# Kernel optimization log

Hardware: AMD Instinct MI355X
Metric: run time of the kernel (lower is better)

## Reference

```python
import jax, jax.numpy as jnp
import numpy as np

B, L, D_MODEL, H = 2, 2048, 2048, 16
HD = D_MODEL // H  # 128 head dim
EPS = 1e-6


def rms_norm(x, scale):
    # float32 RMSNorm over last dim, per Flux QKNorm
    x32 = x.astype(jnp.float32)
    rrms = jax.lax.rsqrt(jnp.mean(x32 * x32, axis=-1, keepdims=True) + EPS)
    return (x32 * rrms) * scale


def apply_rope(xq, xk, freqs_cis):
    # xq, xk: [B, L, H, D]; freqs_cis: [1, L, 1, D/2, 2, 2]
    shp = xq.shape
    xq_ = xq.astype(jnp.float32).reshape(*shp[:-1], -1, 1, 2)
    xk_ = xk.astype(jnp.float32).reshape(*shp[:-1], -1, 1, 2)
    xq_out = freqs_cis[..., 0] * xq_[..., 0] + freqs_cis[..., 1] * xq_[..., 1]
    xk_out = freqs_cis[..., 0] * xk_[..., 0] + freqs_cis[..., 1] * xk_[..., 1]
    return xq_out.reshape(shp).astype(xq.dtype), xk_out.reshape(shp).astype(xk.dtype)


def setup_inputs() -> dict:
    key = jax.random.key(0)
    k1, k2, k3, k4 = jax.random.split(key, 4)
    x = jax.random.normal(k1, (B, L, D_MODEL), dtype=jnp.float32)
    pe = jax.random.normal(k2, (1, L, 1, HD // 2, 2, 2), dtype=jnp.float32)
    w_qkv = jax.random.normal(k3, (D_MODEL, 3 * D_MODEL), dtype=jnp.float32) * (D_MODEL ** -0.5)
    w_proj = jax.random.normal(k4, (D_MODEL, D_MODEL), dtype=jnp.float32) * (D_MODEL ** -0.5)
    q_scale = jnp.ones((HD,), dtype=jnp.float32)
    k_scale = jnp.ones((HD,), dtype=jnp.float32)
    return {"x": x, "pe": pe, "w_qkv": w_qkv, "w_proj": w_proj,
            "q_scale": q_scale, "k_scale": k_scale}


def reference(x, pe, w_qkv, w_proj, q_scale, k_scale):
    qkv = x @ w_qkv                                  # [B, L, 3*H*D]
    qkv = qkv.reshape(B, L, 3, H, HD)
    q, k, v = qkv[:, :, 0], qkv[:, :, 1], qkv[:, :, 2]  # [B, L, H, D]
    # QK RMSNorm (cast back to v's dtype, per QKNorm.forward)
    q = rms_norm(q, q_scale).astype(v.dtype)
    k = rms_norm(k, k_scale).astype(v.dtype)
    # RoPE
    q, k = apply_rope(q, k, pe)
    # non-causal SDPA
    scale = HD ** -0.5
    scores = jnp.einsum('blhd,bmhd->bhlm', q, k) * scale
    attn = jax.nn.softmax(scores, axis=-1)
    out = jnp.einsum('bhlm,bmhd->blhd', attn, v)     # [B, L, H, D]
    out = out.reshape(B, L, H * HD)
    return out @ w_proj
```

## Files before the change

kernel.cpp:

```cpp
#include <hip/hip_runtime.h>

typedef unsigned short u16;
typedef __bf16 bf16x8 __attribute__((ext_vector_type(8)));
typedef float f32x4 __attribute__((ext_vector_type(4)));

#define DEV static __device__ __forceinline__

constexpr int Bc  = 2;
constexpr int Lc  = 2048;
constexpr int Dc  = 2048;
constexpr int Hc  = 16;
constexpr int HDc = 128;
constexpr int Mc  = Bc * Lc;
constexpr int N3c = 3 * Dc;

DEV u16 f2bf(float f) {
  unsigned u = __builtin_bit_cast(unsigned, f);
  u += 0x7fffu + ((u >> 16) & 1u);
  return (u16)(u >> 16);
}
DEV float bf2f(u16 h) { return __builtin_bit_cast(float, ((unsigned)h) << 16); }

DEV void load16(const void* g, void* l) {
  __builtin_amdgcn_global_load_lds(
      (__attribute__((address_space(1))) void*)(g),
      (__attribute__((address_space(3))) void*)(l), 16, 0, 0);
}

__global__ __launch_bounds__(256) void k_prep(const float* __restrict__ x,
                                              const float* __restrict__ w_qkv,
                                              const float* __restrict__ w_proj,
                                              u16* __restrict__ xb,
                                              u16* __restrict__ wqkvT,
                                              u16* __restrict__ wpT) {
  __shared__ u16 t[128 * 136];
  int bid = blockIdx.x;
  int tid = threadIdx.x;
  if (bid < 4096) {
    int i = bid * 256 + tid;
    const float4* s = (const float4*)x;
    float4 a = s[2 * i], b = s[2 * i + 1];
    uint4 o;
    o.x = f2bf(a.x) | ((unsigned)f2bf(a.y) << 16);
    o.y = f2bf(a.z) | ((unsigned)f2bf(a.w) << 16);
    o.z = f2bf(b.x) | ((unsigned)f2bf(b.y) << 16);
    o.w = f2bf(b.z) | ((unsigned)f2bf(b.w) << 16);
    ((uint4*)xb)[i] = o;
    return;
  }
  const float* src;
  u16* dst;
  int tiles_c;
  long ss;
  if (bid < 4096 + 768) {
    int bx = bid - 4096;
    src = w_qkv; dst = wqkvT; tiles_c = 48; ss = N3c;
    int tr = bx / tiles_c, tc = bx % tiles_c;
    src += (long)tr * 128 * ss + tc * 128;
    dst += (long)(tc * 128) * Dc + tr * 128;
  } else {
    int bx = bid - 4864;
    src = w_proj; dst = wpT; tiles_c = 16; ss = Dc;
    int tr = bx / tiles_c, tc = bx % tiles_c;
    src += (long)tr * 128 * ss + tc * 128;
    dst += (long)(tc * 128) * Dc + tr * 128;
  }
#pragma unroll
  for (int p = 0; p < 16; p++) {
    int r = p * 8 + (tid >> 5);
    int c4 = (tid & 31) * 4;
    float4 v = *(const float4*)(src + (long)r * ss + c4);
    t[(c4 + 0) * 136 + r] = f2bf(v.x);
    t[(c4 + 1) * 136 + r] = f2bf(v.y);
    t[(c4 + 2) * 136 + r] = f2bf(v.z);
    t[(c4 + 3) * 136 + r] = f2bf(v.w);
  }
  __syncthreads();
#pragma unroll
  for (int p = 0; p < 8; p++) {
    int c = p * 16 + (tid >> 4);
    int r8 = (tid & 15) * 8;
    uint4 v = *(const uint4*)&t[c * 136 + r8];
    *(uint4*)(dst + (long)c * Dc + r8) = v;
  }
}

__global__ __launch_bounds__(256) void k_vtrans(const u16* __restrict__ qkvb,
                                                u16* __restrict__ Vt) {
  int lt = blockIdx.x;
  int bh = blockIdx.y;
  int b = bh >> 4, h = bh & 15;
  const u16* s = qkvb + (long)(b * Lc + lt * 128) * N3c + 2 * Dc + h * HDc;
  u16* d = Vt + (long)bh * HDc * Lc + lt * 128;
  __shared__ u16 t[128 * 136];
  int tid = threadIdx.x;
#pragma unroll
  for (int p = 0; p < 8; p++) {
    int r = p * 16 + (tid >> 4);
    int c = (tid & 15) * 8;
    uint4 v = *(const uint4*)(s + (long)r * N3c + c);
    const u16* pv = (const u16*)&v;
#pragma unroll
    for (int j = 0; j < 8; j++) t[(c + j) * 136 + r] = pv[j];
  }
  __syncthreads();
#pragma unroll
  for (int p = 0; p < 8; p++) {
    int c = p * 16 + (tid >> 4);
    int r8 = (tid & 15) * 8;
    *(uint4*)(d + (long)c * Lc + r8) = *(const uint4*)&t[c * 136 + r8];
  }
}

DEV void cstore(float* p, float v) { *p = v; }
DEV void cstore(u16* p, float v) { *p = f2bf(v); }

template <typename OT>
__global__ __launch_bounds__(512, 2) void k_gemm2p(const u16* __restrict__ A,
                                                   const u16* __restrict__ Bt,
                                                   OT* __restrict__ C,
                                                   int M, int N, int K,
                                                   int RM, int RC) {
  __shared__ __align__(16) u16 sA[3][128 * 64];
  __shared__ __align__(16) u16 sB[3][256 * 64];

  int nb = N >> 8;
  int x = blockIdx.x & 7;
  int u = blockIdx.x >> 3;
  int rcr = nb / RC;
  int brow = (x / rcr) * RM + (u % RM);
  int bcol = (x % rcr) * RC + (u / RM);

  int tid = threadIdx.x, w = tid >> 6, lane = tid & 63;
  int wm = w >> 2, wn = w & 3;
  int quad = lane >> 4, l15 = lane & 15;
  int lr = lane >> 3, lc = lane & 7;
  int NT = K >> 6;

  const u16* Ag = A + (long)(brow * 128 + w * 8 + lr) * K + (lc ^ lr) * 8;
  const u16* Bg = Bt + (long)(bcol * 256 + w * 8 + lr) * K + (lc ^ lr) * 8;

  f32x4 acc[4][4] = {};
  bf16x8 a[4][2];
  bf16x8 b[4][2];

#define STAGE_A(c, t)                                                          \
  if ((t) < NT) {                                                              \
    _Pragma("unroll") for (int j = 0; j < 2; j++)                              \
        load16(Ag + (long)(j * 64) * K + (long)(t) * 64,                       \
               &sA[c][(j * 64 + w * 8) * 64]);                                 \
  }
#define STAGE_B(c, t)                                                          \
  if ((t) < NT) {                                                              \
    _Pragma("unroll") for (int j = 0; j < 4; j++)                              \
        load16(Bg + (long)(j * 64) * K + (long)(t) * 64,                       \
               &sB[c][(j * 64 + w * 8) * 64]);                                 \
  }
#define LDAB(c)                                                                \
  _Pragma("unroll") for (int mi = 0; mi < 4; mi++) {                           \
    int r = wm * 64 + mi * 16 + l15;                                           \
    _Pragma("unroll") for (int kk = 0; kk < 2; kk++)                           \
        a[mi][kk] =                                                            \
        *(const bf16x8*)&sA[c][r * 64 + (((kk * 4 + quad) ^ (r & 7)) << 3)];   \
  }                                                                            \
  _Pragma("unroll") for (int fi = 0; fi < 4; fi++) {                           \
    int rn = wn * 64 + fi * 16 + l15;                                          \
    _Pragma("unroll") for (int kk = 0; kk < 2; kk++)                           \
        b[fi][kk] =                                                            \
        *(const bf16x8*)&sB[c][rn * 64 + (((kk * 4 + quad) ^ (rn & 7)) << 3)]; \
  }
#define MFMAH(qm)                                                              \
  _Pragma("unroll") for (int mi = 0; mi < 2; mi++)                             \
  _Pragma("unroll") for (int fi = 0; fi < 4; fi++)                             \
  _Pragma("unroll") for (int kk = 0; kk < 2; kk++)                             \
      acc[(qm)*2 + mi][fi] = __builtin_amdgcn_mfma_f32_16x16x32_bf16(          \
          a[(qm)*2 + mi][kk], b[fi][kk], acc[(qm)*2 + mi][fi], 0, 0, 0);
#define BAR() __builtin_amdgcn_s_barrier()
#define LGKM0()                                      \
  asm volatile("s_waitcnt lgkmcnt(0)" ::: "memory"); \
  __builtin_amdgcn_sched_barrier(0)

#define TILE(c, t)                                                             \
  {                                                                            \
    LDAB(c);                                                                   \
    LGKM0();                                                                   \
    __builtin_amdgcn_s_setprio(1);                                             \
    MFMAH(0);                                                                  \
    __builtin_amdgcn_s_setprio(0);                                             \
    BAR();                        \
    STAGE_A(c, (t) + 3);                                                       \
    STAGE_B(c, (t) + 3);                                                       \
    __builtin_amdgcn_s_setprio(1);                                             \
    MFMAH(1);                                                                  \
    __builtin_amdgcn_s_setprio(0);                                             \
    if ((t) < NT - 3) {                                                        \
      asm volatile("s_waitcnt vmcnt(12)" ::: "memory");                        \
    } else if ((t) == NT - 3) {                                                \
      asm volatile("s_waitcnt vmcnt(6)" ::: "memory");                         \
    } else {                                                                   \
      asm volatile("s_waitcnt vmcnt(0)" ::: "memory");                         \
    }                                                                          \
    __builtin_amdgcn_sched_barrier(0);                                         \
    BAR();                          \
  }

  STAGE_A(0, 0);
  STAGE_B(0, 0);
  STAGE_A(1, 1);
  STAGE_B(1, 1);
  STAGE_A(2, 2);
  STAGE_B(2, 2);
  asm volatile("s_waitcnt vmcnt(12)" ::: "memory");
  __builtin_amdgcn_sched_barrier(0);
  BAR();

  int kt = 0;
  for (; kt + 2 < NT; kt += 3) {
    TILE(0, kt);
    TILE(1, kt + 1);
    TILE(2, kt + 2);
  }
  if (kt < NT) { TILE(0, kt); }
  if (kt + 1 < NT) { TILE(1, kt + 1); }

  long orow = (long)brow * 128 + wm * 64;
  int ocol = bcol * 256 + wn * 64;
#pragma unroll
  for (int mi = 0; mi < 4; mi++)
#pragma unroll
    for (int fi = 0; fi < 4; fi++)
#pragma unroll
      for (int r = 0; r < 4; r++)
        cstore(&C[(orow + mi * 16 + quad * 4 + r) * (long)N + ocol + fi * 16 + l15],
               acc[mi][fi][r]);
#undef STAGE_A
#undef STAGE_B
#undef LDAB
#undef MFMAH
#undef BAR
#undef LGKM0
#undef TILE
}

__global__ __launch_bounds__(256) void k_rmsrope(const u16* __restrict__ qkvb,
                                                 const float* __restrict__ pe,
                                                 const float* __restrict__ qsc,
                                                 const float* __restrict__ ksc,
                                                 u16* __restrict__ Qr,
                                                 u16* __restrict__ Kr) {
  int row = blockIdx.x;
  int l = row & (Lc - 1);
  int b = row >> 11;
  int tid = threadIdx.x;
  int h = tid >> 4, s16 = tid & 15;
  int d0 = s16 * 8;
  const u16* qp = qkvb + (long)row * N3c + h * HDc + d0;
  uint4 qv = *(const uint4*)qp;
  uint4 kv = *(const uint4*)(qp + Dc);
  const u16* qu = (const u16*)&qv;
  const u16* ku = (const u16*)&kv;
  float q[8], k[8];
#pragma unroll
  for (int j = 0; j < 8; j++) {
    q[j] = bf2f(qu[j]);
    k[j] = bf2f(ku[j]);
  }
  float sq = 0.f, sk = 0.f;
#pragma unroll
  for (int j = 0; j < 8; j++) {
    sq += q[j] * q[j];
    sk += k[j] * k[j];
  }
#pragma unroll
  for (int m = 1; m < 16; m <<= 1) {
    sq += __shfl_xor(sq, m);
    sk += __shfl_xor(sk, m);
  }
  float rq = rsqrtf(sq * (1.f / HDc) + 1e-6f);
  float rk = rsqrtf(sk * (1.f / HDc) + 1e-6f);
  float qs8[8], ks8[8];
  *(float4*)&qs8[0] = *(const float4*)(qsc + d0);
  *(float4*)&qs8[4] = *(const float4*)(qsc + d0 + 4);
  *(float4*)&ks8[0] = *(const float4*)(ksc + d0);
  *(float4*)&ks8[4] = *(const float4*)(ksc + d0 + 4);
#pragma unroll
  for (int j = 0; j < 8; j++) {
    q[j] *= rq * qs8[j];
    k[j] *= rk * ks8[j];
  }
  float e[16];
  const float* pep = pe + (long)l * 256 + s16 * 16;
#pragma unroll
  for (int j = 0; j < 4; j++) *(float4*)&e[j * 4] = *(const float4*)(pep + j * 4);
  float qo[8], ko[8];
#pragma unroll
  for (int p = 0; p < 4; p++) {
    float e00 = e[p * 4 + 0], e01 = e[p * 4 + 1];
    float e10 = e[p * 4 + 2], e11 = e[p * 4 + 3];
    qo[2 * p]     = e00 * q[2 * p] + e01 * q[2 * p + 1];
    qo[2 * p + 1] = e10 * q[2 * p] + e11 * q[2 * p + 1];
    ko[2 * p]     = e00 * k[2 * p] + e01 * k[2 * p + 1];
    ko[2 * p + 1] = e10 * k[2 * p] + e11 * k[2 * p + 1];
  }
  constexpr float RS = 0.08838834764831845f;
  uint4 oq, ok;
  oq.x = f2bf(qo[0] * RS) | ((unsigned)f2bf(qo[1] * RS) << 16);
  oq.y = f2bf(qo[2] * RS) | ((unsigned)f2bf(qo[3] * RS) << 16);
  oq.z = f2bf(qo[4] * RS) | ((unsigned)f2bf(qo[5] * RS) << 16);
  oq.w = f2bf(qo[6] * RS) | ((unsigned)f2bf(qo[7] * RS) << 16);
  ok.x = f2bf(ko[0]) | ((unsigned)f2bf(ko[1]) << 16);
  ok.y = f2bf(ko[2]) | ((unsigned)f2bf(ko[3]) << 16);
  ok.z = f2bf(ko[4]) | ((unsigned)f2bf(ko[5]) << 16);
  ok.w = f2bf(ko[6]) | ((unsigned)f2bf(ko[7]) << 16);
  long o = (((long)(b * Hc + h)) * Lc + l) * HDc + d0;
  *(uint4*)(Qr + o) = oq;
  *(uint4*)(Kr + o) = ok;
}

__global__ __launch_bounds__(256, 3) void k_attn(const u16* __restrict__ Qr,
                                                 const u16* __restrict__ Kr,
                                                 const u16* __restrict__ Vt,
                                                 u16* __restrict__ Ao) {
  __shared__ u16 smem[24576];
  u16* sQ = smem;
  u16* sK = smem + 8192;
  u16* sV = smem + 16384;
  u16* sP = sQ;
  int bx = blockIdx.x;
  int bh = (bx & 7) | ((bx >> 8) << 3);
  int lt = (bx >> 3) & 31;
  const u16* Qg = Qr + ((long)bh * Lc + lt * 64) * HDc;
  const u16* Kg = Kr + (long)bh * Lc * HDc;
  const u16* Vg = Vt + (long)bh * HDc * Lc;
  int tid = threadIdx.x, w = tid >> 6, lane = tid & 63;
  int quad = lane >> 4, l15 = lane & 15;
  int wsl = w >> 1, wsm = w & 1;
  int wd = w >> 1, wl2 = w & 1;

#pragma unroll
  for (int i = 0; i < 4; i++) {
    int r = i * 16 + w * 4 + quad;
    int gch = l15 ^ (r & 15);
    load16(Qg + (long)r * HDc + gch * 8, sQ + (i * 16 + w * 4) * 128);
  }
  __syncthreads();
  bf16x8 qf[2][4];
#pragma unroll
  for (int mi = 0; mi < 2; mi++) {
    int l = wsl * 32 + mi * 16 + l15;
#pragma unroll
    for (int kk = 0; kk < 4; kk++)
      qf[mi][kk] = *(const bf16x8*)&sQ[l * 128 + (((kk * 4 + quad) ^ l15) << 3)];
  }

  f32x4 o[4][2] = {};
  float rs[8] = {};
  for (int t = 0; t < 32; t++) {
    int m0 = t * 64;
    __syncthreads();
#pragma unroll
    for (int i = 0; i < 4; i++) {
      int r = i * 16 + w * 4 + quad;
      int gch = l15 ^ (r & 15);
      load16(Kg + ((long)(m0 + r)) * HDc + gch * 8, sK + (i * 16 + w * 4) * 128);
    }
#pragma unroll
    for (int i = 0; i < 4; i++) {
      int r = i * 32 + w * 8 + (lane >> 3);
      int gch = (lane & 7) ^ (r & 7);
      load16(Vg + (long)r * Lc + m0 + gch * 8, sV + (i * 32 + w * 8) * 64);
    }
    __syncthreads();
    f32x4 s[2][2] = {};
#pragma unroll
    for (int kk = 0; kk < 4; kk++) {
      bf16x8 bk[2];
#pragma unroll
      for (int ni = 0; ni < 2; ni++) {
        int m = wsm * 32 + ni * 16 + l15;
        bk[ni] = *(const bf16x8*)&sK[m * 128 + (((kk * 4 + quad) ^ l15) << 3)];
      }
#pragma unroll
      for (int mi = 0; mi < 2; mi++)
#pragma unroll
        for (int ni = 0; ni < 2; ni++)
          s[mi][ni] =
              __builtin_amdgcn_mfma_f32_16x16x32_bf16(qf[mi][kk], bk[ni], s[mi][ni], 0, 0, 0);
    }
#pragma unroll
    for (int mi = 0; mi < 2; mi++)
#pragma unroll
      for (int ni = 0; ni < 2; ni++) {
        int pc = wsm * 32 + ni * 16 + l15;
#pragma unroll
        for (int r = 0; r < 4; r++) {
          int pr = wsl * 32 + mi * 16 + quad * 4 + r;
          float p = __expf(s[mi][ni][r]);
          rs[mi * 4 + r] += p;
          unsigned u = __builtin_bit_cast(unsigned, p) + 0x8000u;
          sP[pr * 64 + ((((pc >> 3) ^ (pr & 7)) << 3) | (pc & 7))] = (u16)(u >> 16);
        }
      }
    __syncthreads();
#pragma unroll
    for (int kk = 0; kk < 2; kk++) {
      bf16x8 av[4], bp[2];
#pragma unroll
      for (int mi = 0; mi < 4; mi++) {
        int d = wd * 64 + mi * 16 + l15;
        av[mi] = *(const bf16x8*)&sV[d * 64 + (((kk * 4 + quad) ^ (d & 7)) << 3)];
      }
#pragma unroll
      for (int ni = 0; ni < 2; ni++) {
        int l = wl2 * 32 + ni * 16 + l15;
        bp[ni] = *(const bf16x8*)&sP[l * 64 + (((kk * 4 + quad) ^ (l & 7)) << 3)];
      }
#pragma unroll
      for (int mi = 0; mi < 4; mi++)
#pragma unroll
        for (int ni = 0; ni < 2; ni++)
          o[mi][ni] =
              __builtin_amdgcn_mfma_f32_16x16x32_bf16(av[mi], bp[ni], o[mi][ni], 0, 0, 0);
    }
  }
  __syncthreads();
  float* red  = (float*)sK;
  float* rsum = (float*)sV;
#pragma unroll
  for (int mi = 0; mi < 2; mi++)
#pragma unroll
    for (int r = 0; r < 4; r++) {
      int l = wsl * 32 + mi * 16 + quad * 4 + r;
      red[l * 33 + wsm * 16 + l15] = rs[mi * 4 + r];
    }
  __syncthreads();
  if (tid < 64) {
    float a = 0.f;
#pragma unroll
    for (int j = 0; j < 32; j++) a += red[tid * 33 + j];
    rsum[tid] = a;
  }
  __syncthreads();
  int b = bh >> 4, h = bh & 15;
#pragma unroll
  for (int ni = 0; ni < 2; ni++) {
    int l = wl2 * 32 + ni * 16 + l15;
    float inv = 1.f / rsum[l];
    long rowb = ((long)(b * Lc + lt * 64 + l)) * Dc + h * HDc;
#pragma unroll
    for (int mi = 0; mi < 4; mi++) {
      int d = wd * 64 + mi * 16 + quad * 4;
      ushort4 pk;
      pk.x = f2bf(o[mi][ni][0] * inv);
      pk.y = f2bf(o[mi][ni][1] * inv);
      pk.z = f2bf(o[mi][ni][2] * inv);
      pk.w = f2bf(o[mi][ni][3] * inv);
      *(ushort4*)(Ao + rowb + d) = pk;
    }
  }
}

extern "C" void kernel_launch(void* const* d_in, const int* in_sizes, int n_in,
                              void* d_out, int out_size, void* d_ws, size_t ws_size,
                              hipStream_t stream) {
  const float* x      = (const float*)d_in[0];
  const float* pe     = (const float*)d_in[1];
  const float* w_qkv  = (const float*)d_in[2];
  const float* w_proj = (const float*)d_in[3];
  const float* qs     = (const float*)d_in[4];
  const float* ks     = (const float*)d_in[5];
  float* out = (float*)d_out;
  char* ws = (char*)d_ws;

  u16* xb    = (u16*)(ws);
  u16* wqkvT = (u16*)(ws + 16777216);
  u16* wpT   = (u16*)(ws + 41943040);
  u16* qkvb  = (u16*)(ws + 50331648);
  u16* Qr    = (u16*)(ws + 100663296);
  u16* Kr    = (u16*)(ws + 117440512);
  u16* Vtw   = (u16*)(ws + 134217728);
  u16* Ao    = (u16*)(ws + 150994944);

  k_prep<<<5120, 256, 0, stream>>>(x, w_qkv, w_proj, xb, wqkvT, wpT);
  k_gemm2p<u16><<<32 * 24, 512, 0, stream>>>(xb, wqkvT, qkvb, Mc, N3c, Dc, 16, 6);
  k_rmsrope<<<Mc, 256, 0, stream>>>(qkvb, pe, qs, ks, Qr, Kr);
  k_vtrans<<<dim3(16, 32), 256, 0, stream>>>(qkvb, Vtw);
  k_attn<<<32 * 32, 256, 0, stream>>>(Qr, Kr, Vtw, Ao);
  k_gemm2p<float><<<32 * 8, 512, 0, stream>>>(Ao, wpT, out, Mc, Dc, Dc, 8, 4);
}
```

Baseline: 408.7 us.

## Double-buffer GEMM register fragments to overlap LDS reads with MFMA

Restructures the GEMM main loop so the LDS-to-register fragment loads for the next k-tile are issued while the MFMAs for the current tile run, using two register fragment sets. There is now one barrier per tile instead of two, and the global-to-LDS staging is issued right after that barrier. The goal is to hide LDS read latency and cut barrier stalls. The cost is roughly double the fragment register footprint, which may lower occupancy or cause spills. The tail handling also assumes the tile count parity fits the two-step loop.

```diff
diff --git a/kernel.cpp b/kernel.cpp
--- a/kernel.cpp
+++ b/kernel.cpp
@@ -141,87 +141,90 @@
   const u16* Bg = Bt + (long)(bcol * 256 + w * 8 + lr) * K + (lc ^ lr) * 8;
 
   f32x4 acc[4][4] = {};
-  bf16x8 a[4][2];
-  bf16x8 b[4][2];
-
-#define STAGE_A(c, t)                                                          \
+  bf16x8 a0[4][2], b0[4][2];
+  bf16x8 a1[4][2], b1[4][2];
+
+#define STAGE(c, t)                                                            \
   if ((t) < NT) {                                                              \
     _Pragma("unroll") for (int j = 0; j < 2; j++)                              \
         load16(Ag + (long)(j * 64) * K + (long)(t) * 64,                       \
                &sA[c][(j * 64 + w * 8) * 64]);                                 \
-  }
-#define STAGE_B(c, t)                                                          \
-  if ((t) < NT) {                                                              \
     _Pragma("unroll") for (int j = 0; j < 4; j++)                              \
         load16(Bg + (long)(j * 64) * K + (long)(t) * 64,                       \
                &sB[c][(j * 64 + w * 8) * 64]);                                 \
   }
-#define LDAB(c)                                                                \
+#define LDAB(c, ar, br)                                                        \
   _Pragma("unroll") for (int mi = 0; mi < 4; mi++) {                           \
     int r = wm * 64 + mi * 16 + l15;                                           \
     _Pragma("unroll") for (int kk = 0; kk < 2; kk++)                           \
-        a[mi][kk] =                                                            \
+        ar[mi][kk] =                                                           \
         *(const bf16x8*)&sA[c][r * 64 + (((kk * 4 + quad) ^ (r & 7)) << 3)];   \
   }                                                                            \
   _Pragma("unroll") for (int fi = 0; fi < 4; fi++) {                           \
     int rn = wn * 64 + fi * 16 + l15;                                          \
     _Pragma("unroll") for (int kk = 0; kk < 2; kk++)                           \
-        b[fi][kk] =                                                            \
+        br[fi][kk] =                                                           \
         *(const bf16x8*)&sB[c][rn * 64 + (((kk * 4 + quad) ^ (rn & 7)) << 3)]; \
   }
-#define MFMAH(qm)                                                              \
-  _Pragma("unroll") for (int mi = 0; mi < 2; mi++)                             \
+#define MFMAALL(ar, br)                                                        \
+  _Pragma("unroll") for (int mi = 0; mi < 4; mi++)                             \
   _Pragma("unroll") for (int fi = 0; fi < 4; fi++)                             \
   _Pragma("unroll") for (int kk = 0; kk < 2; kk++)                             \
-      acc[(qm)*2 + mi][fi] = __builtin_amdgcn_mfma_f32_16x16x32_bf16(          \
-          a[(qm)*2 + mi][kk], b[fi][kk], acc[(qm)*2 + mi][fi], 0, 0, 0);
+      acc[mi][fi] = __builtin_amdgcn_mfma_f32_16x16x32_bf16(                   \
+          ar[mi][kk], br[fi][kk], acc[mi][fi], 0, 0, 0);
+#define SB() __builtin_amdgcn_sched_barrier(0)
 #define BAR() __builtin_amdgcn_s_barrier()
-#define LGKM0()                                      \
-  asm volatile("s_waitcnt lgkmcnt(0)" ::: "memory"); \
-  __builtin_amdgcn_sched_barrier(0)
-
-#define TILE(c, t)                                                             \
+#define WAITV(n) asm volatile("s_waitcnt vmcnt(" #n ")" ::: "memory")
+#define WAITL0() asm volatile("s_waitcnt lgkmcnt(0)" ::: "memory")
+
+#define TILE_BODY(tt, sbuf, rbuf, arC, brC, arN, brN, vkeep)                   \
   {                                                                            \
-    LDAB(c);                                                                   \
-    LGKM0();                                                                   \
+    WAITV(vkeep);                                                              \
+    SB();                                                                      \
+    BAR();                                                                     \
+    SB();                                                                      \
+    STAGE(sbuf, (tt) + 3);                                                     \
+    LDAB(rbuf, arN, brN);                                                      \
     __builtin_amdgcn_s_setprio(1);                                             \
-    MFMAH(0);                                                                  \
+    MFMAALL(arC, brC);                                                         \
     __builtin_amdgcn_s_setprio(0);                                             \
-    BAR();                        \
-    STAGE_A(c, (t) + 3);                                                       \
-    STAGE_B(c, (t) + 3);                                                       \
-    __builtin_amdgcn_s_setprio(1);                                             \
-    MFMAH(1);                                                                  \
-    __builtin_amdgcn_s_setprio(0);                                             \
-    if ((t) < NT - 3) {                                                        \
-      asm volatile("s_waitcnt vmcnt(12)" ::: "memory");                        \
-    } else if ((t) == NT - 3) {                                                \
-      asm volatile("s_waitcnt vmcnt(6)" ::: "memory");                         \
-    } else {                                                                   \
-      asm volatile("s_waitcnt vmcnt(0)" ::: "memory");                         \
-    }                                                                          \
-    __builtin_amdgcn_sched_barrier(0);                                         \
-    BAR();                          \
-  }
-
-  STAGE_A(0, 0);
-  STAGE_B(0, 0);
-  STAGE_A(1, 1);
-  STAGE_B(1, 1);
-  STAGE_A(2, 2);
-  STAGE_B(2, 2);
-  asm volatile("s_waitcnt vmcnt(12)" ::: "memory");
-  __builtin_amdgcn_sched_barrier(0);
+    WAITL0();                                                                  \
+  }
+
+  STAGE(0, 0);
+  STAGE(1, 1);
+  STAGE(2, 2);
+  WAITV(12);
+  SB();
   BAR();
-
-  int kt = 0;
-  for (; kt + 2 < NT; kt += 3) {
-    TILE(0, kt);
-    TILE(1, kt + 1);
-    TILE(2, kt + 2);
-  }
-  if (kt < NT) { TILE(0, kt); }
-  if (kt + 1 < NT) { TILE(1, kt + 1); }
+  SB();
+  LDAB(0, a0, b0);
+  WAITL0();
+
+  int si = 0, ri = 1;
+  int t = 0;
+  for (; t < NT - 2; t += 2) {
+    TILE_BODY(t, si, ri, a0, b0, a1, b1, 6);
+    si = si == 2 ? 0 : si + 1;
+    ri = ri == 2 ? 0 : ri + 1;
+    TILE_BODY(t + 1, si, ri, a1, b1, a0, b0, 6);
+    si = si == 2 ? 0 : si + 1;
+    ri = ri == 2 ? 0 : ri + 1;
+  }
+  {
+    WAITV(0);
+    SB();
+    BAR();
+    SB();
+    LDAB(ri, a1, b1);
+    __builtin_amdgcn_s_setprio(1);
+    MFMAALL(a0, b0);
+    __builtin_amdgcn_s_setprio(0);
+    WAITL0();
+  }
+  __builtin_amdgcn_s_setprio(1);
+  MFMAALL(a1, b1);
+  __builtin_amdgcn_s_setprio(0);
 
   long orow = (long)brow * 128 + wm * 64;
   int ocol = bcol * 256 + wn * 64;
@@ -233,13 +236,14 @@
       for (int r = 0; r < 4; r++)
         cstore(&C[(orow + mi * 16 + quad * 4 + r) * (long)N + ocol + fi * 16 + l15],
                acc[mi][fi][r]);
-#undef STAGE_A
-#undef STAGE_B
+#undef STAGE
 #undef LDAB
-#undef MFMAH
+#undef MFMAALL
+#undef SB
 #undef BAR
-#undef LGKM0
-#undef TILE
+#undef WAITV
+#undef WAITL0
+#undef TILE_BODY
 }
 
 __global__ __launch_bounds__(256) void k_rmsrope(const u16* __restrict__ qkvb,
```

New measurement: 440.4 us. 1.08x slower.

## Prefetch next K/V tile during PV phase of attention loop

Applied to the files above, without the earlier changes.

The attention kernel now issues the next iteration's K tile load (global-to-LDS) and the V tile load (into registers) right after the P tile is written, so the loads overlap with the P·V MFMA work. The V registers are then stored to LDS at the start of the next iteration. This hides global load latency behind compute, but holds V in extra registers, and the K prefetch overwrites sK while nothing else reads it. Whether the async K load needs an explicit wait before the next barrier is not visible here.

```diff
diff --git a/kernel.cpp b/kernel.cpp
--- a/kernel.cpp
+++ b/kernel.cpp
@@ -337,6 +337,14 @@
   int wsl = w >> 1, wsm = w & 1;
   int wd = w >> 1, wl2 = w & 1;
 
+  int vrr0 = w * 8 + (lane >> 3);
+  int vg0 = (lane & 7) ^ (vrr0 & 7);
+  const u16* Vg0 = Vg + (long)(vrr0 + 0)  * Lc + vg0 * 8;
+  const u16* Vg1 = Vg + (long)(vrr0 + 32) * Lc + vg0 * 8;
+  const u16* Vg2 = Vg + (long)(vrr0 + 64) * Lc + vg0 * 8;
+  const u16* Vg3 = Vg + (long)(vrr0 + 96) * Lc + vg0 * 8;
+  u16* sVw = sV + (w * 8) * 64 + lane * 8;
+
 #pragma unroll
   for (int i = 0; i < 4; i++) {
     int r = i * 16 + w * 4 + quad;
@@ -352,24 +360,27 @@
     for (int kk = 0; kk < 4; kk++)
       qf[mi][kk] = *(const bf16x8*)&sQ[l * 128 + (((kk * 4 + quad) ^ l15) << 3)];
   }
+
+#pragma unroll
+  for (int i = 0; i < 4; i++) {
+    int r = i * 16 + w * 4 + quad;
+    int gch = l15 ^ (r & 15);
+    load16(Kg + (long)r * HDc + gch * 8, sK + (i * 16 + w * 4) * 128);
+  }
+  uint4 vr0 = *(const uint4*)(Vg0);
+  uint4 vr1 = *(const uint4*)(Vg1);
+  uint4 vr2 = *(const uint4*)(Vg2);
+  uint4 vr3 = *(const uint4*)(Vg3);
 
   f32x4 o[4][2] = {};
   float rs[8] = {};
   for (int t = 0; t < 32; t++) {
     int m0 = t * 64;
     __syncthreads();
-#pragma unroll
-    for (int i = 0; i < 4; i++) {
-      int r = i * 16 + w * 4 + quad;
-      int gch = l15 ^ (r & 15);
-      load16(Kg + ((long)(m0 + r)) * HDc + gch * 8, sK + (i * 16 + w * 4) * 128);
-    }
-#pragma unroll
-    for (int i = 0; i < 4; i++) {
-      int r = i * 32 + w * 8 + (lane >> 3);
-      int gch = (lane & 7) ^ (r & 7);
-      load16(Vg + (long)r * Lc + m0 + gch * 8, sV + (i * 32 + w * 8) * 64);
-    }
+    *(uint4*)(sVw + 0 * 32 * 64) = vr0;
+    *(uint4*)(sVw + 1 * 32 * 64) = vr1;
+    *(uint4*)(sVw + 2 * 32 * 64) = vr2;
+    *(uint4*)(sVw + 3 * 32 * 64) = vr3;
     __syncthreads();
     f32x4 s[2][2] = {};
 #pragma unroll
@@ -402,6 +413,19 @@
         }
       }
     __syncthreads();
+    if (t + 1 < 32) {
+      int m1 = m0 + 64;
+#pragma unroll
+      for (int i = 0; i < 4; i++) {
+        int r = i * 16 + w * 4 + quad;
+        int gch = l15 ^ (r & 15);
+        load16(Kg + ((long)(m1 + r)) * HDc + gch * 8, sK + (i * 16 + w * 4) * 128);
+      }
+      vr0 = *(const uint4*)(Vg0 + m1);
+      vr1 = *(const uint4*)(Vg1 + m1);
+      vr2 = *(const uint4*)(Vg2 + m1);
+      vr3 = *(const uint4*)(Vg3 + m1);
+    }
 #pragma unroll
     for (int kk = 0; kk < 2; kk++) {
       bf16x8 av[4], bp[2];
```

Result: no change. 408.4 us (-0.1%).
